# Kernel optimization log

Measured on AMD Instinct MI355X. Metric: run time of the kernel, lower is better.

## Reference

```python
import jax, jax.numpy as jnp
import numpy as np

N_NODES = 100000


def gcn_conv(x, edge_index, W, b):
    """PyG GCNConv: h = x @ W; out = D^-1/2 (A+I) D^-1/2 h + b."""
    n = x.shape[0]
    src, dst = edge_index[0], edge_index[1]
    loop = jnp.arange(n)
    src = jnp.concatenate([src, loop])  # add self-loops
    dst = jnp.concatenate([dst, loop])
    # degree at target nodes (unit edge weights)
    deg = jax.ops.segment_sum(jnp.ones(dst.shape[0], dtype=x.dtype), dst, num_segments=n)
    dinv = jnp.where(deg > 0, jax.lax.rsqrt(deg), 0.0)
    norm = dinv[src] * dinv[dst]  # [E+n]
    h = x @ W  # [n, out]
    msg = h[src] * norm[:, None]  # gather + scale
    out = jax.ops.segment_sum(msg, dst, num_segments=n)  # scatter-add
    return out + b


def setup_inputs() -> dict:
    key = jax.random.key(0)
    k1, k2, k3, k4, k5, k6 = jax.random.split(key, 6)
    E = 3200000
    x = jax.random.normal(k1, (N_NODES, 2), dtype=jnp.float32)
    edge_index = jax.random.randint(k2, (2, E), 0, N_NODES, dtype=jnp.int64)
    W1 = jax.random.normal(k3, (2, 16), dtype=jnp.float32) * 0.5
    b1 = jax.random.normal(k4, (16,), dtype=jnp.float32) * 0.1
    W2 = jax.random.normal(k5, (16, 2), dtype=jnp.float32) * 0.25
    b2 = jax.random.normal(k6, (2,), dtype=jnp.float32) * 0.1
    return {"x": x, "edge_index": edge_index, "W1": W1, "b1": b1, "W2": W2, "b2": b2}


def reference(x, edge_index, W1, b1, W2, b2):
    h = jax.nn.relu(gcn_conv(x, edge_index, W1, b1))
    # dropout is identity at inference
    out = gcn_conv(h, edge_index, W2, b2)
    return jax.nn.log_softmax(out, axis=1)
```

## Files before the change

### kernel.cpp

```cpp
#include <hip/hip_runtime.h>
#include <math.h>


constexpr int N = 100000;
constexpr int LOGCB = 10;
constexpr int CB = 1 << LOGCB;
constexpr int NC = 98;
constexpr int CAP1 = 35008;

constexpr int B1 = 512;
constexpr int EC1 = 8192;
constexpr int EPT1 = EC1 / B1;

constexpr int BA = 256;
constexpr int ECA = 2048;
constexpr int EPTA = ECA / BA;
constexpr int MAXCH = (CAP1 + ECA - 1) / ECA;

__global__ __launch_bounds__(B1) void k_pass1(const int* __restrict__ src,
                                              const int* __restrict__ dst, int E,
                                              int* __restrict__ gfill1,
                                              int* __restrict__ slotsC) {
    __shared__ int hist[NC];
    __shared__ int base[NC];
    int t = threadIdx.x;
    if (t < NC) hist[t] = 0;
    __syncthreads();
    int s[EPT1], d[EPT1];
    int ebase = blockIdx.x * EC1 + t * EPT1;
#pragma unroll
    for (int k = 0; k < EPT1 / 4; k++) {
        int idx = ebase + 4 * k;
        if (idx + 3 < E) {
            *(int4*)(s + 4 * k) = *(const int4*)(src + idx);
            *(int4*)(d + 4 * k) = *(const int4*)(dst + idx);
        } else {
            for (int j = 0; j < 4; j++) {
                s[4 * k + j] = (idx + j < E) ? src[idx + j] : -1;
                d[4 * k + j] = (idx + j < E) ? dst[idx + j] : -1;
            }
        }
    }
#pragma unroll
    for (int k = 0; k < EPT1; k++)
        if (d[k] >= 0) atomicAdd(&hist[d[k] >> LOGCB], 1);
    __syncthreads();
    if (t < NC) {
        int c = hist[t];
        base[t] = c ? atomicAdd(&gfill1[t], c) : 0;
        hist[t] = 0;
    }
    __syncthreads();
#pragma unroll
    for (int k = 0; k < EPT1; k++) {
        if (d[k] >= 0) {
            int bin = d[k] >> LOGCB;
            int r = atomicAdd(&hist[bin], 1);
            int pos = base[bin] + r;
            if (pos < CAP1) slotsC[bin * CAP1 + pos] = (s[k] << LOGCB) | (d[k] & (CB - 1));
        }
    }
}

__global__ __launch_bounds__(BA) void k_deg(const int* __restrict__ gfill1,
                                            const int* __restrict__ slotsC,
                                            int* __restrict__ degPart) {
    __shared__ int dh[CB];
    int c = blockIdx.x / MAXCH, j = blockIdx.x % MAXCH;
    int fill = min(gfill1[c], CAP1);
    int e0 = j * ECA;
    if (e0 >= fill) return;
    int e1 = min(fill, e0 + ECA);
    int t = threadIdx.x;
    for (int i = t; i < CB; i += BA) dh[i] = 0;
    __syncthreads();
    const int* row = slotsC + c * CAP1;
    int v[EPTA];
    int ebase = e0 + t * EPTA;
#pragma unroll
    for (int k = 0; k < EPTA / 4; k++) {
        int idx = ebase + 4 * k;
        if (idx + 3 < e1) {
            *(int4*)(v + 4 * k) = *(const int4*)(row + idx);
        } else {
            for (int jj = 0; jj < 4; jj++) v[4 * k + jj] = (idx + jj < e1) ? row[idx + jj] : -1;
        }
    }
#pragma unroll
    for (int k = 0; k < EPTA; k++)
        if (v[k] >= 0) atomicAdd(&dh[v[k] & (CB - 1)], 1);
    __syncthreads();
    int* dp = degPart + blockIdx.x * CB;
    for (int i = t; i < CB; i += BA) dp[i] = dh[i];
}

__global__ __launch_bounds__(256) void k_dinv(const int* __restrict__ gfill1,
                                              const int* __restrict__ degPart,
                                              const float* __restrict__ x,
                                              float* __restrict__ dinv,
                                              float2* __restrict__ sx) {
    int node = blockIdx.x * 256 + threadIdx.x;
    if (node >= N) return;
    int c = node >> LOGCB, i = node & (CB - 1);
    int nch = (min(gfill1[c], CAP1) + ECA - 1) / ECA;
    const int* p = degPart + (size_t)c * MAXCH * CB + i;
    int deg = 0;
    for (int j = 0; j < nch; j++) deg += p[j * CB];
    float di = rsqrtf((float)(deg + 1));
    dinv[node] = di;
    float2 xv = ((const float2*)x)[node];
    sx[node] = make_float2(xv.x * di, xv.y * di);
}

__global__ __launch_bounds__(BA) void k_aggc(const int* __restrict__ gfill1,
                                             const int* __restrict__ slotsC,
                                             const float2* __restrict__ vals,
                                             float* __restrict__ partX,
                                             float* __restrict__ partY) {
    __shared__ float aX[CB], aY[CB];
    int c = blockIdx.x / MAXCH, j = blockIdx.x % MAXCH;
    int fill = min(gfill1[c], CAP1);
    int e0 = j * ECA;
    if (e0 >= fill) return;
    int e1 = min(fill, e0 + ECA);
    int t = threadIdx.x;
    for (int i = t; i < CB; i += BA) { aX[i] = 0.f; aY[i] = 0.f; }
    __syncthreads();
    const int* row = slotsC + c * CAP1;
    int v[EPTA];
    int ebase = e0 + t * EPTA;
#pragma unroll
    for (int k = 0; k < EPTA / 4; k++) {
        int idx = ebase + 4 * k;
        if (idx + 3 < e1) {
            *(int4*)(v + 4 * k) = *(const int4*)(row + idx);
        } else {
            for (int jj = 0; jj < 4; jj++) v[4 * k + jj] = (idx + jj < e1) ? row[idx + jj] : -1;
        }
    }
    float2 g[EPTA];
#pragma unroll
    for (int k = 0; k < EPTA; k++) g[k] = (v[k] >= 0) ? vals[v[k] >> LOGCB] : make_float2(0.f, 0.f);
#pragma unroll
    for (int k = 0; k < EPTA; k++) {
        if (v[k] >= 0) {
            int d = v[k] & (CB - 1);
            atomicAdd(&aX[d], g[k].x);
            atomicAdd(&aY[d], g[k].y);
        }
    }
    __syncthreads();
    float* px = partX + blockIdx.x * CB;
    float* py = partY + blockIdx.x * CB;
    for (int i = t; i < CB; i += BA) { px[i] = aX[i]; py[i] = aY[i]; }
}

__global__ __launch_bounds__(256) void k_comb1(const int* __restrict__ gfill1,
                                               const float* __restrict__ partX,
                                               const float* __restrict__ partY,
                                               const float* __restrict__ dinv,
                                               const float2* __restrict__ sx,
                                               const float* __restrict__ W1,
                                               const float* __restrict__ b1,
                                               const float* __restrict__ W2,
                                               float2* __restrict__ sz) {
    __shared__ float sW1[32], sb1[16], sW2[32];
    int t = threadIdx.x;
    if (t < 32) sW1[t] = W1[t];
    else if (t < 48) sb1[t - 32] = b1[t - 32];
    else if (t < 80) sW2[t - 48] = W2[t - 48];
    __syncthreads();
    int node = blockIdx.x * 256 + t;
    if (node >= N) return;
    int c = node >> LOGCB, i = node & (CB - 1);
    int nch = (min(gfill1[c], CAP1) + ECA - 1) / ECA;
    const float* px = partX + (size_t)c * MAXCH * CB + i;
    const float* py = partY + (size_t)c * MAXCH * CB + i;
    float ax = 0.f, ay = 0.f;
    for (int j = 0; j < nch; j++) { ax += px[j * CB]; ay += py[j * CB]; }
    float di = dinv[node];
    float2 sv = sx[node];
    float a0 = (ax + sv.x) * di;
    float a1 = (ay + sv.y) * di;
    float z0 = 0.f, z1 = 0.f;
#pragma unroll
    for (int k = 0; k < 16; k++) {
        float h = fmaf(a0, sW1[k], fmaf(a1, sW1[16 + k], sb1[k]));
        h = fmaxf(h, 0.f);
        z0 = fmaf(h, sW2[2 * k + 0], z0);
        z1 = fmaf(h, sW2[2 * k + 1], z1);
    }
    sz[node] = make_float2(z0 * di, z1 * di);
}

__global__ __launch_bounds__(256) void k_comb2(const int* __restrict__ gfill1,
                                               const float* __restrict__ partX,
                                               const float* __restrict__ partY,
                                               const float* __restrict__ dinv,
                                               const float2* __restrict__ sz,
                                               const float* __restrict__ b2,
                                               float2* __restrict__ out) {
    int node = blockIdx.x * 256 + threadIdx.x;
    if (node >= N) return;
    int c = node >> LOGCB, i = node & (CB - 1);
    int nch = (min(gfill1[c], CAP1) + ECA - 1) / ECA;
    const float* px = partX + (size_t)c * MAXCH * CB + i;
    const float* py = partY + (size_t)c * MAXCH * CB + i;
    float ax = 0.f, ay = 0.f;
    for (int j = 0; j < nch; j++) { ax += px[j * CB]; ay += py[j * CB]; }
    float di = dinv[node];
    float2 sv = sz[node];
    float v0 = fmaf(ax + sv.x, di, b2[0]);
    float v1 = fmaf(ay + sv.y, di, b2[1]);
    float m = fmaxf(v0, v1);
    float lse = m + logf(expf(v0 - m) + expf(v1 - m));
    out[node] = make_float2(v0 - lse, v1 - lse);
}

extern "C" void kernel_launch(void* const* d_in, const int* in_sizes, int n_in,
                              void* d_out, int out_size, void* d_ws, size_t ws_size,
                              hipStream_t stream) {
    const float* x  = (const float*)d_in[0];
    const int*   ei = (const int*)d_in[1];
    const float* W1 = (const float*)d_in[2];
    const float* b1 = (const float*)d_in[3];
    const float* W2 = (const float*)d_in[4];
    const float* b2 = (const float*)d_in[5];

    const int E = in_sizes[1] / 2;
    const int* src = ei;
    const int* dst = ei + E;
    const int GP = (E + EC1 - 1) / EC1;
    const int GB = NC * MAXCH;
    const int GN = (N + 255) / 256;

    char* ws = (char*)d_ws;
    size_t off = 0;
    auto alloc = [&](size_t bytes) {
        char* p = ws + off;
        off += (bytes + 511) & ~size_t(511);
        return p;
    };
    int*    gfill1  = (int*)alloc(128 * sizeof(int));
    float*  dinv    = (float*)alloc(N * sizeof(float));
    float2* sx      = (float2*)alloc(N * sizeof(float2));
    float2* sz      = (float2*)alloc(N * sizeof(float2));
    int*    slotsC  = (int*)alloc((size_t)NC * CAP1 * sizeof(int));
    int*    degPart = (int*)alloc((size_t)GB * CB * sizeof(int));
    float*  partX   = (float*)alloc((size_t)GB * CB * sizeof(float));
    float*  partY   = (float*)alloc((size_t)GB * CB * sizeof(float));

    hipMemsetAsync(gfill1, 0, 128 * sizeof(int), stream);

    k_pass1<<<GP, B1, 0, stream>>>(src, dst, E, gfill1, slotsC);
    k_deg<<<GB, BA, 0, stream>>>(gfill1, slotsC, degPart);
    k_dinv<<<GN, 256, 0, stream>>>(gfill1, degPart, x, dinv, sx);
    k_aggc<<<GB, BA, 0, stream>>>(gfill1, slotsC, sx, partX, partY);
    k_comb1<<<GN, 256, 0, stream>>>(gfill1, partX, partY, dinv, sx, W1, b1, W2, sz);
    k_aggc<<<GB, BA, 0, stream>>>(gfill1, slotsC, sz, partX, partY);
    k_comb2<<<GN, 256, 0, stream>>>(gfill1, partX, partY, dinv, sz, b2, (float2*)d_out);
}
```

Before: 214.7 us.

## Split fused gather-scatter aggregation into separate gather and scatter kernels

The combined gather-plus-shared-atomic aggregation kernel is split in two. One kernel gathers the source values per edge into a contiguous message buffer, and a second kernel streams those messages and does the shared-memory atomic scatter. The aim is to separate latency-bound random gathers from LDS atomic contention so each phase can reach better occupancy and memory-level parallelism. The cost is an extra write and read of an edge-sized float2 buffer (about 27 MB) and two more launches. The degree partials also now alias the partX buffer to save workspace.

```diff
diff --git a/kernel.cpp b/kernel.cpp
--- a/kernel.cpp
+++ b/kernel.cpp
@@ -112,9 +112,46 @@
     sx[node] = make_float2(xv.x * di, xv.y * di);
 }
 
-__global__ __launch_bounds__(BA) void k_aggc(const int* __restrict__ gfill1,
+__global__ __launch_bounds__(BA) void k_gath(const int* __restrict__ gfill1,
                                              const int* __restrict__ slotsC,
                                              const float2* __restrict__ vals,
+                                             float2* __restrict__ msg) {
+    int c = blockIdx.x / MAXCH, j = blockIdx.x % MAXCH;
+    int fill = min(gfill1[c], CAP1);
+    int e0 = j * ECA;
+    if (e0 >= fill) return;
+    int e1 = min(fill, e0 + ECA);
+    int t = threadIdx.x;
+    const int* row = slotsC + c * CAP1;
+    float2* mrow = msg + (size_t)c * CAP1;
+    int v[EPTA];
+    int ebase = e0 + t * EPTA;
+#pragma unroll
+    for (int k = 0; k < EPTA / 4; k++) {
+        int idx = ebase + 4 * k;
+        if (idx + 3 < e1) {
+            *(int4*)(v + 4 * k) = *(const int4*)(row + idx);
+        } else {
+            for (int jj = 0; jj < 4; jj++) v[4 * k + jj] = (idx + jj < e1) ? row[idx + jj] : -1;
+        }
+    }
+    float2 g[EPTA];
+#pragma unroll
+    for (int k = 0; k < EPTA; k++) g[k] = (v[k] >= 0) ? vals[v[k] >> LOGCB] : make_float2(0.f, 0.f);
+#pragma unroll
+    for (int k = 0; k < EPTA; k += 2) {
+        int idx = ebase + k;
+        if (idx + 1 < e1) {
+            *(float4*)(mrow + idx) = make_float4(g[k].x, g[k].y, g[k + 1].x, g[k + 1].y);
+        } else if (idx < e1) {
+            mrow[idx] = g[k];
+        }
+    }
+}
+
+__global__ __launch_bounds__(BA) void k_scat(const int* __restrict__ gfill1,
+                                             const int* __restrict__ slotsC,
+                                             const float2* __restrict__ msg,
                                              float* __restrict__ partX,
                                              float* __restrict__ partY) {
     __shared__ float aX[CB], aY[CB];
@@ -127,7 +164,9 @@
     for (int i = t; i < CB; i += BA) { aX[i] = 0.f; aY[i] = 0.f; }
     __syncthreads();
     const int* row = slotsC + c * CAP1;
+    const float2* mrow = msg + (size_t)c * CAP1;
     int v[EPTA];
+    float2 m[EPTA];
     int ebase = e0 + t * EPTA;
 #pragma unroll
     for (int k = 0; k < EPTA / 4; k++) {
@@ -138,15 +177,24 @@
             for (int jj = 0; jj < 4; jj++) v[4 * k + jj] = (idx + jj < e1) ? row[idx + jj] : -1;
         }
     }
-    float2 g[EPTA];
-#pragma unroll
-    for (int k = 0; k < EPTA; k++) g[k] = (v[k] >= 0) ? vals[v[k] >> LOGCB] : make_float2(0.f, 0.f);
+#pragma unroll
+    for (int k = 0; k < EPTA; k += 2) {
+        int idx = ebase + k;
+        if (idx + 1 < e1) {
+            float4 p = *(const float4*)(mrow + idx);
+            m[k] = make_float2(p.x, p.y);
+            m[k + 1] = make_float2(p.z, p.w);
+        } else {
+            m[k] = (idx < e1) ? mrow[idx] : make_float2(0.f, 0.f);
+            m[k + 1] = make_float2(0.f, 0.f);
+        }
+    }
 #pragma unroll
     for (int k = 0; k < EPTA; k++) {
         if (v[k] >= 0) {
             int d = v[k] & (CB - 1);
-            atomicAdd(&aX[d], g[k].x);
-            atomicAdd(&aY[d], g[k].y);
+            atomicAdd(&aX[d], m[k].x);
+            atomicAdd(&aY[d], m[k].y);
         }
     }
     __syncthreads();
@@ -241,22 +289,25 @@
         off += (bytes + 511) & ~size_t(511);
         return p;
     };
-    int*    gfill1  = (int*)alloc(128 * sizeof(int));
-    float*  dinv    = (float*)alloc(N * sizeof(float));
-    float2* sx      = (float2*)alloc(N * sizeof(float2));
-    float2* sz      = (float2*)alloc(N * sizeof(float2));
-    int*    slotsC  = (int*)alloc((size_t)NC * CAP1 * sizeof(int));
-    int*    degPart = (int*)alloc((size_t)GB * CB * sizeof(int));
-    float*  partX   = (float*)alloc((size_t)GB * CB * sizeof(float));
-    float*  partY   = (float*)alloc((size_t)GB * CB * sizeof(float));
+    int*    gfill1 = (int*)alloc(128 * sizeof(int));
+    float*  dinv   = (float*)alloc(N * sizeof(float));
+    float2* sx     = (float2*)alloc(N * sizeof(float2));
+    float2* sz     = (float2*)alloc(N * sizeof(float2));
+    int*    slotsC = (int*)alloc((size_t)NC * CAP1 * sizeof(int));
+    float2* msg    = (float2*)alloc((size_t)NC * CAP1 * sizeof(float2));
+    float*  partX  = (float*)alloc((size_t)GB * CB * sizeof(float));
+    float*  partY  = (float*)alloc((size_t)GB * CB * sizeof(float));
+    int*    degPart = (int*)partX;
 
     hipMemsetAsync(gfill1, 0, 128 * sizeof(int), stream);
 
     k_pass1<<<GP, B1, 0, stream>>>(src, dst, E, gfill1, slotsC);
     k_deg<<<GB, BA, 0, stream>>>(gfill1, slotsC, degPart);
     k_dinv<<<GN, 256, 0, stream>>>(gfill1, degPart, x, dinv, sx);
-    k_aggc<<<GB, BA, 0, stream>>>(gfill1, slotsC, sx, partX, partY);
+    k_gath<<<GB, BA, 0, stream>>>(gfill1, slotsC, sx, msg);
+    k_scat<<<GB, BA, 0, stream>>>(gfill1, slotsC, msg, partX, partY);
     k_comb1<<<GN, 256, 0, stream>>>(gfill1, partX, partY, dinv, sx, W1, b1, W2, sz);
-    k_aggc<<<GB, BA, 0, stream>>>(gfill1, slotsC, sz, partX, partY);
+    k_gath<<<GB, BA, 0, stream>>>(gfill1, slotsC, sz, msg);
+    k_scat<<<GB, BA, 0, stream>>>(gfill1, slotsC, msg, partX, partY);
     k_comb2<<<GN, 256, 0, stream>>>(gfill1, partX, partY, dinv, sz, b2, (float2*)d_out);
 }
```

Result: slower. 264.3 us (+23.1%).

## Fuse all GCN stages into one persistent kernel with software grid barriers

Applied to the files above, without the earlier changes.

Replaces the seven kernel launches (binning pass, degree histogram, dinv, two aggregations, two combines) with a single persistent kernel of 1024 blocks. The stages are separated by an atomic counter/sense grid barrier, and the blocks loop over work units. The shared-memory buffers of the stages are unioned, and the bucketing pass now uses 4096-edge chunks on 256 threads. The aim is to remove launch gaps and inter-kernel drain, at the cost of spin-wait barriers. The scheme relies on all 1024 blocks being co-resident; if they are not, it deadlocks.

```diff
diff --git a/kernel.cpp b/kernel.cpp
--- a/kernel.cpp
+++ b/kernel.cpp
@@ -8,213 +8,232 @@
 constexpr int NC = 98;
 constexpr int CAP1 = 35008;
 
-constexpr int B1 = 512;
-constexpr int EC1 = 8192;
-constexpr int EPT1 = EC1 / B1;
-
-constexpr int BA = 256;
+constexpr int NBLK = 1024;
+constexpr int BT = 256;
+
+constexpr int EC0 = 4096;
+constexpr int EPT0 = EC0 / BT;
 constexpr int ECA = 2048;
-constexpr int EPTA = ECA / BA;
+constexpr int EPTA = ECA / BT;
 constexpr int MAXCH = (CAP1 + ECA - 1) / ECA;
-
-__global__ __launch_bounds__(B1) void k_pass1(const int* __restrict__ src,
-                                              const int* __restrict__ dst, int E,
-                                              int* __restrict__ gfill1,
-                                              int* __restrict__ slotsC) {
-    __shared__ int hist[NC];
-    __shared__ int base[NC];
+constexpr int NUNIT = NC * MAXCH;
+
+struct SMem {
+    union {
+        struct { int hist[NC]; int base[NC]; } p0;
+        int dh[CB];
+        struct { float aX[CB]; float aY[CB]; } ag;
+        float w[CB];
+    };
+};
+
+__device__ __forceinline__ void gridbar(int* cnt, int* sense, int phase) {
+    __syncthreads();
+    if (threadIdx.x == 0) {
+        __threadfence();
+        int prev = atomicAdd(&cnt[phase], 1);
+        if (prev == NBLK - 1) {
+            __hip_atomic_store(sense, phase + 1, __ATOMIC_RELAXED, __HIP_MEMORY_SCOPE_AGENT);
+        } else {
+            while (__hip_atomic_load(sense, __ATOMIC_RELAXED, __HIP_MEMORY_SCOPE_AGENT) <= phase)
+                __builtin_amdgcn_s_sleep(2);
+        }
+        __threadfence();
+    }
+    __syncthreads();
+}
+
+__device__ __forceinline__ void agg_walk(SMem& sm, const int* gfill1,
+                                         const int* slotsC, const float2* vals,
+                                         float* partX, float* partY) {
     int t = threadIdx.x;
-    if (t < NC) hist[t] = 0;
+    for (int u = blockIdx.x; u < NUNIT; u += NBLK) {
+        int c = u / MAXCH, j = u % MAXCH;
+        int fill = min(gfill1[c], CAP1);
+        int e0 = j * ECA;
+        if (e0 >= fill) continue;
+        int e1 = min(fill, e0 + ECA);
+        for (int i = t; i < CB; i += BT) { sm.ag.aX[i] = 0.f; sm.ag.aY[i] = 0.f; }
+        __syncthreads();
+        const int* row = slotsC + c * CAP1;
+        int v[EPTA];
+        int ebase = e0 + t * EPTA;
+#pragma unroll
+        for (int k = 0; k < EPTA / 4; k++) {
+            int idx = ebase + 4 * k;
+            if (idx + 3 < e1) {
+                *(int4*)(v + 4 * k) = *(const int4*)(row + idx);
+            } else {
+                for (int jj = 0; jj < 4; jj++) v[4 * k + jj] = (idx + jj < e1) ? row[idx + jj] : -1;
+            }
+        }
+        float2 g[EPTA];
+#pragma unroll
+        for (int k = 0; k < EPTA; k++)
+            g[k] = (v[k] >= 0) ? vals[v[k] >> LOGCB] : make_float2(0.f, 0.f);
+#pragma unroll
+        for (int k = 0; k < EPTA; k++) {
+            if (v[k] >= 0) {
+                int d = v[k] & (CB - 1);
+                atomicAdd(&sm.ag.aX[d], g[k].x);
+                atomicAdd(&sm.ag.aY[d], g[k].y);
+            }
+        }
+        __syncthreads();
+        float* px = partX + (size_t)u * CB;
+        float* py = partY + (size_t)u * CB;
+        for (int i = t; i < CB; i += BT) { px[i] = sm.ag.aX[i]; py[i] = sm.ag.aY[i]; }
+        __syncthreads();
+    }
+}
+
+__global__ __launch_bounds__(BT, 4) void k_fused(
+    const int* __restrict__ src, const int* __restrict__ dst, int E, int nch0,
+    const float* __restrict__ x, const float* __restrict__ W1,
+    const float* __restrict__ b1, const float* __restrict__ W2,
+    const float* __restrict__ b2, int* __restrict__ bar, int* __restrict__ gfill1,
+    int* __restrict__ slotsC, int* __restrict__ degPart, float* __restrict__ partX,
+    float* __restrict__ partY, float* __restrict__ dinv, float2* __restrict__ sx,
+    float2* __restrict__ sz, float2* __restrict__ out) {
+    __shared__ SMem sm;
+    int t = threadIdx.x;
+    int* cnt = bar;
+    int* sense = bar + 8;
+
+    if ((int)blockIdx.x < nch0) {
+        if (t < NC) sm.p0.hist[t] = 0;
+        __syncthreads();
+        int s[EPT0], d[EPT0];
+        int ebase = blockIdx.x * EC0 + t * EPT0;
+#pragma unroll
+        for (int k = 0; k < EPT0 / 4; k++) {
+            int idx = ebase + 4 * k;
+            if (idx + 3 < E) {
+                *(int4*)(s + 4 * k) = *(const int4*)(src + idx);
+                *(int4*)(d + 4 * k) = *(const int4*)(dst + idx);
+            } else {
+                for (int j = 0; j < 4; j++) {
+                    s[4 * k + j] = (idx + j < E) ? src[idx + j] : -1;
+                    d[4 * k + j] = (idx + j < E) ? dst[idx + j] : -1;
+                }
+            }
+        }
+#pragma unroll
+        for (int k = 0; k < EPT0; k++)
+            if (d[k] >= 0) atomicAdd(&sm.p0.hist[d[k] >> LOGCB], 1);
+        __syncthreads();
+        if (t < NC) {
+            int c = sm.p0.hist[t];
+            sm.p0.base[t] = c ? atomicAdd(&gfill1[t], c) : 0;
+            sm.p0.hist[t] = 0;
+        }
+        __syncthreads();
+#pragma unroll
+        for (int k = 0; k < EPT0; k++) {
+            if (d[k] >= 0) {
+                int bin = d[k] >> LOGCB;
+                int r = atomicAdd(&sm.p0.hist[bin], 1);
+                int pos = sm.p0.base[bin] + r;
+                if (pos < CAP1) slotsC[bin * CAP1 + pos] = (s[k] << LOGCB) | (d[k] & (CB - 1));
+            }
+        }
+    }
+    gridbar(cnt, sense, 0);
+
+    for (int u = blockIdx.x; u < NUNIT; u += NBLK) {
+        int c = u / MAXCH, j = u % MAXCH;
+        int fill = min(gfill1[c], CAP1);
+        int e0 = j * ECA;
+        if (e0 >= fill) continue;
+        int e1 = min(fill, e0 + ECA);
+        for (int i = t; i < CB; i += BT) sm.dh[i] = 0;
+        __syncthreads();
+        const int* row = slotsC + c * CAP1;
+        int v[EPTA];
+        int ebase = e0 + t * EPTA;
+#pragma unroll
+        for (int k = 0; k < EPTA / 4; k++) {
+            int idx = ebase + 4 * k;
+            if (idx + 3 < e1) {
+                *(int4*)(v + 4 * k) = *(const int4*)(row + idx);
+            } else {
+                for (int jj = 0; jj < 4; jj++) v[4 * k + jj] = (idx + jj < e1) ? row[idx + jj] : -1;
+            }
+        }
+#pragma unroll
+        for (int k = 0; k < EPTA; k++)
+            if (v[k] >= 0) atomicAdd(&sm.dh[v[k] & (CB - 1)], 1);
+        __syncthreads();
+        int* dp = degPart + (size_t)u * CB;
+        for (int i = t; i < CB; i += BT) dp[i] = sm.dh[i];
+        __syncthreads();
+    }
+    gridbar(cnt, sense, 1);
+
+    for (int node = blockIdx.x * BT + t; node < N; node += NBLK * BT) {
+        int c = node >> LOGCB, i = node & (CB - 1);
+        int nch = (min(gfill1[c], CAP1) + ECA - 1) / ECA;
+        const int* p = degPart + (size_t)c * MAXCH * CB + i;
+        int deg = 0;
+        for (int j = 0; j < nch; j++) deg += p[j * CB];
+        float di = rsqrtf((float)(deg + 1));
+        dinv[node] = di;
+        float2 xv = ((const float2*)x)[node];
+        sx[node] = make_float2(xv.x * di, xv.y * di);
+    }
+    gridbar(cnt, sense, 2);
+
+    agg_walk(sm, gfill1, slotsC, sx, partX, partY);
+    gridbar(cnt, sense, 3);
+
+    if (t < 80) {
+        sm.w[t] = (t < 32) ? W1[t] : (t < 48) ? b1[t - 32] : W2[t - 48];
+    }
     __syncthreads();
-    int s[EPT1], d[EPT1];
-    int ebase = blockIdx.x * EC1 + t * EPT1;
-#pragma unroll
-    for (int k = 0; k < EPT1 / 4; k++) {
-        int idx = ebase + 4 * k;
-        if (idx + 3 < E) {
-            *(int4*)(s + 4 * k) = *(const int4*)(src + idx);
-            *(int4*)(d + 4 * k) = *(const int4*)(dst + idx);
-        } else {
-            for (int j = 0; j < 4; j++) {
-                s[4 * k + j] = (idx + j < E) ? src[idx + j] : -1;
-                d[4 * k + j] = (idx + j < E) ? dst[idx + j] : -1;
-            }
-        }
-    }
-#pragma unroll
-    for (int k = 0; k < EPT1; k++)
-        if (d[k] >= 0) atomicAdd(&hist[d[k] >> LOGCB], 1);
-    __syncthreads();
-    if (t < NC) {
-        int c = hist[t];
-        base[t] = c ? atomicAdd(&gfill1[t], c) : 0;
-        hist[t] = 0;
-    }
-    __syncthreads();
-#pragma unroll
-    for (int k = 0; k < EPT1; k++) {
-        if (d[k] >= 0) {
-            int bin = d[k] >> LOGCB;
-            int r = atomicAdd(&hist[bin], 1);
-            int pos = base[bin] + r;
-            if (pos < CAP1) slotsC[bin * CAP1 + pos] = (s[k] << LOGCB) | (d[k] & (CB - 1));
-        }
-    }
-}
-
-__global__ __launch_bounds__(BA) void k_deg(const int* __restrict__ gfill1,
-                                            const int* __restrict__ slotsC,
-                                            int* __restrict__ degPart) {
-    __shared__ int dh[CB];
-    int c = blockIdx.x / MAXCH, j = blockIdx.x % MAXCH;
-    int fill = min(gfill1[c], CAP1);
-    int e0 = j * ECA;
-    if (e0 >= fill) return;
-    int e1 = min(fill, e0 + ECA);
-    int t = threadIdx.x;
-    for (int i = t; i < CB; i += BA) dh[i] = 0;
-    __syncthreads();
-    const int* row = slotsC + c * CAP1;
-    int v[EPTA];
-    int ebase = e0 + t * EPTA;
-#pragma unroll
-    for (int k = 0; k < EPTA / 4; k++) {
-        int idx = ebase + 4 * k;
-        if (idx + 3 < e1) {
-            *(int4*)(v + 4 * k) = *(const int4*)(row + idx);
-        } else {
-            for (int jj = 0; jj < 4; jj++) v[4 * k + jj] = (idx + jj < e1) ? row[idx + jj] : -1;
-        }
-    }
-#pragma unroll
-    for (int k = 0; k < EPTA; k++)
-        if (v[k] >= 0) atomicAdd(&dh[v[k] & (CB - 1)], 1);
-    __syncthreads();
-    int* dp = degPart + blockIdx.x * CB;
-    for (int i = t; i < CB; i += BA) dp[i] = dh[i];
-}
-
-__global__ __launch_bounds__(256) void k_dinv(const int* __restrict__ gfill1,
-                                              const int* __restrict__ degPart,
-                                              const float* __restrict__ x,
-                                              float* __restrict__ dinv,
-                                              float2* __restrict__ sx) {
-    int node = blockIdx.x * 256 + threadIdx.x;
-    if (node >= N) return;
-    int c = node >> LOGCB, i = node & (CB - 1);
-    int nch = (min(gfill1[c], CAP1) + ECA - 1) / ECA;
-    const int* p = degPart + (size_t)c * MAXCH * CB + i;
-    int deg = 0;
-    for (int j = 0; j < nch; j++) deg += p[j * CB];
-    float di = rsqrtf((float)(deg + 1));
-    dinv[node] = di;
-    float2 xv = ((const float2*)x)[node];
-    sx[node] = make_float2(xv.x * di, xv.y * di);
-}
-
-__global__ __launch_bounds__(BA) void k_aggc(const int* __restrict__ gfill1,
-                                             const int* __restrict__ slotsC,
-                                             const float2* __restrict__ vals,
-                                             float* __restrict__ partX,
-                                             float* __restrict__ partY) {
-    __shared__ float aX[CB], aY[CB];
-    int c = blockIdx.x / MAXCH, j = blockIdx.x % MAXCH;
-    int fill = min(gfill1[c], CAP1);
-    int e0 = j * ECA;
-    if (e0 >= fill) return;
-    int e1 = min(fill, e0 + ECA);
-    int t = threadIdx.x;
-    for (int i = t; i < CB; i += BA) { aX[i] = 0.f; aY[i] = 0.f; }
-    __syncthreads();
-    const int* row = slotsC + c * CAP1;
-    int v[EPTA];
-    int ebase = e0 + t * EPTA;
-#pragma unroll
-    for (int k = 0; k < EPTA / 4; k++) {
-        int idx = ebase + 4 * k;
-        if (idx + 3 < e1) {
-            *(int4*)(v + 4 * k) = *(const int4*)(row + idx);
-        } else {
-            for (int jj = 0; jj < 4; jj++) v[4 * k + jj] = (idx + jj < e1) ? row[idx + jj] : -1;
-        }
-    }
-    float2 g[EPTA];
-#pragma unroll
-    for (int k = 0; k < EPTA; k++) g[k] = (v[k] >= 0) ? vals[v[k] >> LOGCB] : make_float2(0.f, 0.f);
-#pragma unroll
-    for (int k = 0; k < EPTA; k++) {
-        if (v[k] >= 0) {
-            int d = v[k] & (CB - 1);
-            atomicAdd(&aX[d], g[k].x);
-            atomicAdd(&aY[d], g[k].y);
-        }
-    }
-    __syncthreads();
-    float* px = partX + blockIdx.x * CB;
-    float* py = partY + blockIdx.x * CB;
-    for (int i = t; i < CB; i += BA) { px[i] = aX[i]; py[i] = aY[i]; }
-}
-
-__global__ __launch_bounds__(256) void k_comb1(const int* __restrict__ gfill1,
-                                               const float* __restrict__ partX,
-                                               const float* __restrict__ partY,
-                                               const float* __restrict__ dinv,
-                                               const float2* __restrict__ sx,
-                                               const float* __restrict__ W1,
-                                               const float* __restrict__ b1,
-                                               const float* __restrict__ W2,
-                                               float2* __restrict__ sz) {
-    __shared__ float sW1[32], sb1[16], sW2[32];
-    int t = threadIdx.x;
-    if (t < 32) sW1[t] = W1[t];
-    else if (t < 48) sb1[t - 32] = b1[t - 32];
-    else if (t < 80) sW2[t - 48] = W2[t - 48];
-    __syncthreads();
-    int node = blockIdx.x * 256 + t;
-    if (node >= N) return;
-    int c = node >> LOGCB, i = node & (CB - 1);
-    int nch = (min(gfill1[c], CAP1) + ECA - 1) / ECA;
-    const float* px = partX + (size_t)c * MAXCH * CB + i;
-    const float* py = partY + (size_t)c * MAXCH * CB + i;
-    float ax = 0.f, ay = 0.f;
-    for (int j = 0; j < nch; j++) { ax += px[j * CB]; ay += py[j * CB]; }
-    float di = dinv[node];
-    float2 sv = sx[node];
-    float a0 = (ax + sv.x) * di;
-    float a1 = (ay + sv.y) * di;
-    float z0 = 0.f, z1 = 0.f;
-#pragma unroll
-    for (int k = 0; k < 16; k++) {
-        float h = fmaf(a0, sW1[k], fmaf(a1, sW1[16 + k], sb1[k]));
-        h = fmaxf(h, 0.f);
-        z0 = fmaf(h, sW2[2 * k + 0], z0);
-        z1 = fmaf(h, sW2[2 * k + 1], z1);
-    }
-    sz[node] = make_float2(z0 * di, z1 * di);
-}
-
-__global__ __launch_bounds__(256) void k_comb2(const int* __restrict__ gfill1,
-                                               const float* __restrict__ partX,
-                                               const float* __restrict__ partY,
-                                               const float* __restrict__ dinv,
-                                               const float2* __restrict__ sz,
-                                               const float* __restrict__ b2,
-                                               float2* __restrict__ out) {
-    int node = blockIdx.x * 256 + threadIdx.x;
-    if (node >= N) return;
-    int c = node >> LOGCB, i = node & (CB - 1);
-    int nch = (min(gfill1[c], CAP1) + ECA - 1) / ECA;
-    const float* px = partX + (size_t)c * MAXCH * CB + i;
-    const float* py = partY + (size_t)c * MAXCH * CB + i;
-    float ax = 0.f, ay = 0.f;
-    for (int j = 0; j < nch; j++) { ax += px[j * CB]; ay += py[j * CB]; }
-    float di = dinv[node];
-    float2 sv = sz[node];
-    float v0 = fmaf(ax + sv.x, di, b2[0]);
-    float v1 = fmaf(ay + sv.y, di, b2[1]);
-    float m = fmaxf(v0, v1);
-    float lse = m + logf(expf(v0 - m) + expf(v1 - m));
-    out[node] = make_float2(v0 - lse, v1 - lse);
+    for (int node = blockIdx.x * BT + t; node < N; node += NBLK * BT) {
+        int c = node >> LOGCB, i = node & (CB - 1);
+        int nch = (min(gfill1[c], CAP1) + ECA - 1) / ECA;
+        const float* px = partX + (size_t)c * MAXCH * CB + i;
+        const float* py = partY + (size_t)c * MAXCH * CB + i;
+        float ax = 0.f, ay = 0.f;
+        for (int j = 0; j < nch; j++) { ax += px[j * CB]; ay += py[j * CB]; }
+        float di = dinv[node];
+        float2 sv = sx[node];
+        float a0 = (ax + sv.x) * di;
+        float a1 = (ay + sv.y) * di;
+        float z0 = 0.f, z1 = 0.f;
+#pragma unroll
+        for (int k = 0; k < 16; k++) {
+            float h = fmaf(a0, sm.w[k], fmaf(a1, sm.w[16 + k], sm.w[32 + k]));
+            h = fmaxf(h, 0.f);
+            z0 = fmaf(h, sm.w[48 + 2 * k + 0], z0);
+            z1 = fmaf(h, sm.w[48 + 2 * k + 1], z1);
+        }
+        sz[node] = make_float2(z0 * di, z1 * di);
+    }
+    gridbar(cnt, sense, 4);
+
+    agg_walk(sm, gfill1, slotsC, sz, partX, partY);
+    gridbar(cnt, sense, 5);
+
+    {
+        float bb0 = b2[0], bb1 = b2[1];
+        for (int node = blockIdx.x * BT + t; node < N; node += NBLK * BT) {
+            int c = node >> LOGCB, i = node & (CB - 1);
+            int nch = (min(gfill1[c], CAP1) + ECA - 1) / ECA;
+            const float* px = partX + (size_t)c * MAXCH * CB + i;
+            const float* py = partY + (size_t)c * MAXCH * CB + i;
+            float ax = 0.f, ay = 0.f;
+            for (int j = 0; j < nch; j++) { ax += px[j * CB]; ay += py[j * CB]; }
+            float di = dinv[node];
+            float2 sv = sz[node];
+            float v0 = fmaf(ax + sv.x, di, bb0);
+            float v1 = fmaf(ay + sv.y, di, bb1);
+            float m = fmaxf(v0, v1);
+            float lse = m + logf(expf(v0 - m) + expf(v1 - m));
+            out[node] = make_float2(v0 - lse, v1 - lse);
+        }
+    }
 }
 
 extern "C" void kernel_launch(void* const* d_in, const int* in_sizes, int n_in,
@@ -230,9 +249,7 @@
     const int E = in_sizes[1] / 2;
     const int* src = ei;
     const int* dst = ei + E;
-    const int GP = (E + EC1 - 1) / EC1;
-    const int GB = NC * MAXCH;
-    const int GN = (N + 255) / 256;
+    const int nch0 = (E + EC0 - 1) / EC0;
 
     char* ws = (char*)d_ws;
     size_t off = 0;
@@ -241,22 +258,19 @@
         off += (bytes + 511) & ~size_t(511);
         return p;
     };
+    int*    bar     = (int*)alloc(16 * sizeof(int));
     int*    gfill1  = (int*)alloc(128 * sizeof(int));
     float*  dinv    = (float*)alloc(N * sizeof(float));
     float2* sx      = (float2*)alloc(N * sizeof(float2));
     float2* sz      = (float2*)alloc(N * sizeof(float2));
     int*    slotsC  = (int*)alloc((size_t)NC * CAP1 * sizeof(int));
-    int*    degPart = (int*)alloc((size_t)GB * CB * sizeof(int));
-    float*  partX   = (float*)alloc((size_t)GB * CB * sizeof(float));
-    float*  partY   = (float*)alloc((size_t)GB * CB * sizeof(float));
-
-    hipMemsetAsync(gfill1, 0, 128 * sizeof(int), stream);
-
-    k_pass1<<<GP, B1, 0, stream>>>(src, dst, E, gfill1, slotsC);
-    k_deg<<<GB, BA, 0, stream>>>(gfill1, slotsC, degPart);
-    k_dinv<<<GN, 256, 0, stream>>>(gfill1, degPart, x, dinv, sx);
-    k_aggc<<<GB, BA, 0, stream>>>(gfill1, slotsC, sx, partX, partY);
-    k_comb1<<<GN, 256, 0, stream>>>(gfill1, partX, partY, dinv, sx, W1, b1, W2, sz);
-    k_aggc<<<GB, BA, 0, stream>>>(gfill1, slotsC, sz, partX, partY);
-    k_comb2<<<GN, 256, 0, stream>>>(gfill1, partX, partY, dinv, sz, b2, (float2*)d_out);
-}
+    int*    degPart = (int*)alloc((size_t)NUNIT * CB * sizeof(int));
+    float*  partX   = (float*)alloc((size_t)NUNIT * CB * sizeof(float));
+    float*  partY   = (float*)alloc((size_t)NUNIT * CB * sizeof(float));
+
+    hipMemsetAsync(bar, 0, 512 + 128 * sizeof(int), stream);
+
+    k_fused<<<NBLK, BT, 0, stream>>>(src, dst, E, nch0, x, W1, b1, W2, b2,
+                                     bar, gfill1, slotsC, degPart, partX, partY,
+                                     dinv, sx, sz, (float2*)d_out);
+}
```

New measurement: 843.1 us. 3.93x slower.

## Assign one wavefront per edge chunk and halve destination bin size

Applied to the files above, without the earlier changes.

The degree and aggregation kernels now give each 64-lane wavefront its own LDS histogram and edge chunk, with eight independent wavefronts per 512-thread block, so no block-wide __syncthreads is needed. Destination bins shrink from 1024 to 512 nodes and chunks to 1024 edges, with the bin count and per-bin capacity recomputed to match. The aim is less barrier stalling, less LDS zeroing and flushing per chunk, and better load balance. The costs are more per-chunk partial slices and more work per lane, and the code relies on wavefront lockstep ordering of LDS accesses.

```diff
diff --git a/kernel.cpp b/kernel.cpp
--- a/kernel.cpp
+++ b/kernel.cpp
@@ -3,19 +3,20 @@
 
 
 constexpr int N = 100000;
-constexpr int LOGCB = 10;
+constexpr int LOGCB = 9;
 constexpr int CB = 1 << LOGCB;
-constexpr int NC = 98;
-constexpr int CAP1 = 35008;
+constexpr int NC = (N + CB - 1) / CB;
+constexpr int ECW = 1024;
+constexpr int MAXCH = 18;
+constexpr int CAP1 = MAXCH * ECW;
+constexpr int EPL = ECW / 64;
+constexpr int NUNIT = NC * MAXCH;
+constexpr int WPB = 8;
+constexpr int GW = NUNIT / WPB;
 
 constexpr int B1 = 512;
 constexpr int EC1 = 8192;
 constexpr int EPT1 = EC1 / B1;
-
-constexpr int BA = 256;
-constexpr int ECA = 2048;
-constexpr int EPTA = ECA / BA;
-constexpr int MAXCH = (CAP1 + ECA - 1) / ECA;
 
 __global__ __launch_bounds__(B1) void k_pass1(const int* __restrict__ src,
                                               const int* __restrict__ dst, int E,
@@ -62,23 +63,24 @@
     }
 }
 
-__global__ __launch_bounds__(BA) void k_deg(const int* __restrict__ gfill1,
-                                            const int* __restrict__ slotsC,
-                                            int* __restrict__ degPart) {
-    __shared__ int dh[CB];
-    int c = blockIdx.x / MAXCH, j = blockIdx.x % MAXCH;
+__global__ __launch_bounds__(512) void k_degw(const int* __restrict__ gfill1,
+                                              const int* __restrict__ slotsC,
+                                              int* __restrict__ degPart) {
+    __shared__ int dh[WPB][CB];
+    int w = threadIdx.x >> 6, lane = threadIdx.x & 63;
+    int u = blockIdx.x * WPB + w;
+    int c = u / MAXCH, j = u % MAXCH;
     int fill = min(gfill1[c], CAP1);
-    int e0 = j * ECA;
+    int e0 = j * ECW;
     if (e0 >= fill) return;
-    int e1 = min(fill, e0 + ECA);
-    int t = threadIdx.x;
-    for (int i = t; i < CB; i += BA) dh[i] = 0;
-    __syncthreads();
+    int e1 = min(fill, e0 + ECW);
+    int* h = dh[w];
+    for (int i = lane; i < CB; i += 64) h[i] = 0;
     const int* row = slotsC + c * CAP1;
-    int v[EPTA];
-    int ebase = e0 + t * EPTA;
-#pragma unroll
-    for (int k = 0; k < EPTA / 4; k++) {
+    int v[EPL];
+    int ebase = e0 + lane * EPL;
+#pragma unroll
+    for (int k = 0; k < EPL / 4; k++) {
         int idx = ebase + 4 * k;
         if (idx + 3 < e1) {
             *(int4*)(v + 4 * k) = *(const int4*)(row + idx);
@@ -87,11 +89,10 @@
         }
     }
 #pragma unroll
-    for (int k = 0; k < EPTA; k++)
-        if (v[k] >= 0) atomicAdd(&dh[v[k] & (CB - 1)], 1);
-    __syncthreads();
-    int* dp = degPart + blockIdx.x * CB;
-    for (int i = t; i < CB; i += BA) dp[i] = dh[i];
+    for (int k = 0; k < EPL; k++)
+        if (v[k] >= 0) atomicAdd(&h[v[k] & (CB - 1)], 1);
+    int* dp = degPart + (size_t)u * CB;
+    for (int i = lane; i < CB; i += 64) dp[i] = h[i];
 }
 
 __global__ __launch_bounds__(256) void k_dinv(const int* __restrict__ gfill1,
@@ -102,7 +103,7 @@
     int node = blockIdx.x * 256 + threadIdx.x;
     if (node >= N) return;
     int c = node >> LOGCB, i = node & (CB - 1);
-    int nch = (min(gfill1[c], CAP1) + ECA - 1) / ECA;
+    int nch = (min(gfill1[c], CAP1) + ECW - 1) / ECW;
     const int* p = degPart + (size_t)c * MAXCH * CB + i;
     int deg = 0;
     for (int j = 0; j < nch; j++) deg += p[j * CB];
@@ -112,25 +113,27 @@
     sx[node] = make_float2(xv.x * di, xv.y * di);
 }
 
-__global__ __launch_bounds__(BA) void k_aggc(const int* __restrict__ gfill1,
-                                             const int* __restrict__ slotsC,
-                                             const float2* __restrict__ vals,
-                                             float* __restrict__ partX,
-                                             float* __restrict__ partY) {
-    __shared__ float aX[CB], aY[CB];
-    int c = blockIdx.x / MAXCH, j = blockIdx.x % MAXCH;
+__global__ __launch_bounds__(512) void k_aggw(const int* __restrict__ gfill1,
+                                              const int* __restrict__ slotsC,
+                                              const float2* __restrict__ vals,
+                                              float* __restrict__ partX,
+                                              float* __restrict__ partY) {
+    __shared__ float aX[WPB][CB], aY[WPB][CB];
+    int w = threadIdx.x >> 6, lane = threadIdx.x & 63;
+    int u = blockIdx.x * WPB + w;
+    int c = u / MAXCH, j = u % MAXCH;
     int fill = min(gfill1[c], CAP1);
-    int e0 = j * ECA;
+    int e0 = j * ECW;
     if (e0 >= fill) return;
-    int e1 = min(fill, e0 + ECA);
-    int t = threadIdx.x;
-    for (int i = t; i < CB; i += BA) { aX[i] = 0.f; aY[i] = 0.f; }
-    __syncthreads();
+    int e1 = min(fill, e0 + ECW);
+    float* ax = aX[w];
+    float* ay = aY[w];
+    for (int i = lane; i < CB; i += 64) { ax[i] = 0.f; ay[i] = 0.f; }
     const int* row = slotsC + c * CAP1;
-    int v[EPTA];
-    int ebase = e0 + t * EPTA;
-#pragma unroll
-    for (int k = 0; k < EPTA / 4; k++) {
+    int v[EPL];
+    int ebase = e0 + lane * EPL;
+#pragma unroll
+    for (int k = 0; k < EPL / 4; k++) {
         int idx = ebase + 4 * k;
         if (idx + 3 < e1) {
             *(int4*)(v + 4 * k) = *(const int4*)(row + idx);
@@ -138,21 +141,21 @@
             for (int jj = 0; jj < 4; jj++) v[4 * k + jj] = (idx + jj < e1) ? row[idx + jj] : -1;
         }
     }
-    float2 g[EPTA];
-#pragma unroll
-    for (int k = 0; k < EPTA; k++) g[k] = (v[k] >= 0) ? vals[v[k] >> LOGCB] : make_float2(0.f, 0.f);
-#pragma unroll
-    for (int k = 0; k < EPTA; k++) {
+    float2 g[EPL];
+#pragma unroll
+    for (int k = 0; k < EPL; k++)
+        g[k] = (v[k] >= 0) ? vals[v[k] >> LOGCB] : make_float2(0.f, 0.f);
+#pragma unroll
+    for (int k = 0; k < EPL; k++) {
         if (v[k] >= 0) {
             int d = v[k] & (CB - 1);
-            atomicAdd(&aX[d], g[k].x);
-            atomicAdd(&aY[d], g[k].y);
-        }
-    }
-    __syncthreads();
-    float* px = partX + blockIdx.x * CB;
-    float* py = partY + blockIdx.x * CB;
-    for (int i = t; i < CB; i += BA) { px[i] = aX[i]; py[i] = aY[i]; }
+            atomicAdd(&ax[d], g[k].x);
+            atomicAdd(&ay[d], g[k].y);
+        }
+    }
+    float* px = partX + (size_t)u * CB;
+    float* py = partY + (size_t)u * CB;
+    for (int i = lane; i < CB; i += 64) { px[i] = ax[i]; py[i] = ay[i]; }
 }
 
 __global__ __launch_bounds__(256) void k_comb1(const int* __restrict__ gfill1,
@@ -173,7 +176,7 @@
     int node = blockIdx.x * 256 + t;
     if (node >= N) return;
     int c = node >> LOGCB, i = node & (CB - 1);
-    int nch = (min(gfill1[c], CAP1) + ECA - 1) / ECA;
+    int nch = (min(gfill1[c], CAP1) + ECW - 1) / ECW;
     const float* px = partX + (size_t)c * MAXCH * CB + i;
     const float* py = partY + (size_t)c * MAXCH * CB + i;
     float ax = 0.f, ay = 0.f;
@@ -203,7 +206,7 @@
     int node = blockIdx.x * 256 + threadIdx.x;
     if (node >= N) return;
     int c = node >> LOGCB, i = node & (CB - 1);
-    int nch = (min(gfill1[c], CAP1) + ECA - 1) / ECA;
+    int nch = (min(gfill1[c], CAP1) + ECW - 1) / ECW;
     const float* px = partX + (size_t)c * MAXCH * CB + i;
     const float* py = partY + (size_t)c * MAXCH * CB + i;
     float ax = 0.f, ay = 0.f;
@@ -231,7 +234,6 @@
     const int* src = ei;
     const int* dst = ei + E;
     const int GP = (E + EC1 - 1) / EC1;
-    const int GB = NC * MAXCH;
     const int GN = (N + 255) / 256;
 
     char* ws = (char*)d_ws;
@@ -241,22 +243,22 @@
         off += (bytes + 511) & ~size_t(511);
         return p;
     };
-    int*    gfill1  = (int*)alloc(128 * sizeof(int));
+    int*    gfill1  = (int*)alloc(256 * sizeof(int));
     float*  dinv    = (float*)alloc(N * sizeof(float));
     float2* sx      = (float2*)alloc(N * sizeof(float2));
     float2* sz      = (float2*)alloc(N * sizeof(float2));
     int*    slotsC  = (int*)alloc((size_t)NC * CAP1 * sizeof(int));
-    int*    degPart = (int*)alloc((size_t)GB * CB * sizeof(int));
-    float*  partX   = (float*)alloc((size_t)GB * CB * sizeof(float));
-    float*  partY   = (float*)alloc((size_t)GB * CB * sizeof(float));
-
-    hipMemsetAsync(gfill1, 0, 128 * sizeof(int), stream);
+    int*    degPart = (int*)alloc((size_t)NUNIT * CB * sizeof(int));
+    float*  partX   = (float*)alloc((size_t)NUNIT * CB * sizeof(float));
+    float*  partY   = (float*)alloc((size_t)NUNIT * CB * sizeof(float));
+
+    hipMemsetAsync(gfill1, 0, 256 * sizeof(int), stream);
 
     k_pass1<<<GP, B1, 0, stream>>>(src, dst, E, gfill1, slotsC);
-    k_deg<<<GB, BA, 0, stream>>>(gfill1, slotsC, degPart);
+    k_degw<<<GW, 512, 0, stream>>>(gfill1, slotsC, degPart);
     k_dinv<<<GN, 256, 0, stream>>>(gfill1, degPart, x, dinv, sx);
-    k_aggc<<<GB, BA, 0, stream>>>(gfill1, slotsC, sx, partX, partY);
+    k_aggw<<<GW, 512, 0, stream>>>(gfill1, slotsC, sx, partX, partY);
     k_comb1<<<GN, 256, 0, stream>>>(gfill1, partX, partY, dinv, sx, W1, b1, W2, sz);
-    k_aggc<<<GB, BA, 0, stream>>>(gfill1, slotsC, sz, partX, partY);
+    k_aggw<<<GW, 512, 0, stream>>>(gfill1, slotsC, sz, partX, partY);
     k_comb2<<<GN, 256, 0, stream>>>(gfill1, partX, partY, dinv, sz, b2, (float2*)d_out);
 }
```

Result: slower. 231.8 us (+7.9%).
